# Kernel tuning notes

Hardware: AMD Instinct MI355X
Metric: run time of the kernel (lower is better)

Reference implementation:

```python
import jax, jax.numpy as jnp
import numpy as np
from jax import lax

HEADS, DIM_HEAD, KSZ = 8, 64, 3


def conv1x1(x, w):
    # x: [B, Cin, X, Y], w: [Cout, Cin]
    return jnp.einsum('oi,bixy->boxy', w, x)


def setup_inputs() -> dict:
    key = jax.random.key(0)
    ks = jax.random.split(key, 8)
    dim = 256
    inner = HEADS * DIM_HEAD  # 512
    B, H, W = 4, 64, 64
    s = 0.02
    return {
        'fmap': jax.random.normal(ks[0], (B, dim, H, W), jnp.float32),
        'w_lin_q': jax.random.normal(ks[1], (inner, dim), jnp.float32) * s,
        'w_lin_kv_dw': jax.random.normal(ks[2], (dim, 1, 3, 3), jnp.float32) * s,
        'w_lin_kv_pw': jax.random.normal(ks[3], (2 * inner, dim), jnp.float32) * s,
        'w_q': jax.random.normal(ks[4], (inner, dim), jnp.float32) * s,
        'w_kv': jax.random.normal(ks[5], (2 * inner, dim), jnp.float32) * s,
        'w_out': jax.random.normal(ks[6], (dim, 2 * inner), jnp.float32) * s,
        'b_out': jax.random.normal(ks[7], (dim,), jnp.float32) * s,
    }


def reference(fmap, w_lin_q, w_lin_kv_dw, w_lin_kv_pw, w_q, w_kv, w_out, b_out):
    B, dim, X, Y = fmap.shape
    h, d, ksz = HEADS, DIM_HEAD, KSZ
    scale = d ** -0.5
    n = X * Y

    # ---- linear (global) attention branch ----
    # depthwise 3x3 conv (groups=dim) then pointwise 1x1, both bias-free
    dw = lax.conv_general_dilated(
        fmap, w_lin_kv_dw, window_strides=(1, 1), padding=[(1, 1), (1, 1)],
        dimension_numbers=('NCHW', 'OIHW', 'NCHW'), feature_group_count=dim)
    lin_kv = conv1x1(dw, w_lin_kv_pw)
    lin_q = conv1x1(fmap, w_lin_q)
    lin_k, lin_v = jnp.split(lin_kv, 2, axis=1)

    def to_bhnd(t):  # [B, h*d, X, Y] -> [B, h, n, d]
        return t.reshape(B, h, d, n).transpose(0, 1, 3, 2)

    lq, lk, lv = to_bhnd(lin_q), to_bhnd(lin_k), to_bhnd(lin_v)
    lq = jax.nn.softmax(lq, axis=-1) * scale   # softmax over feature dim
    lk = jax.nn.softmax(lk, axis=-2)           # softmax over sequence dim
    ctx = jnp.einsum('bhnd,bhne->bhde', lk, lv)
    lin_out = jnp.einsum('bhnd,bhde->bhne', lq, ctx)
    lin_out = lin_out.transpose(0, 1, 3, 2).reshape(B, h * d, X, Y)
    lin_out = jax.nn.gelu(lin_out, approximate=False)  # torch nn.GELU (exact erf)

    # ---- local window attention branch (unfold equivalent) ----
    q = conv1x1(fmap, w_q).reshape(B, h, d, X, Y) * scale
    kv = conv1x1(fmap, w_kv)
    k, v = jnp.split(kv, 2, axis=1)
    k = k.reshape(B, h, d, X, Y)
    v = v.reshape(B, h, d, X, Y)
    pad = ksz // 2
    padw = ((0, 0), (0, 0), (0, 0), (pad, pad), (pad, pad))
    kp = jnp.pad(k, padw)  # zero padding, as in F.unfold
    vp = jnp.pad(v, padw)
    # j enumerates kernel offsets row-major (ky, kx) -> matches F.unfold layout
    k_win = jnp.stack([kp[..., i:i + X, j:j + Y]
                       for i in range(ksz) for j in range(ksz)], axis=2)  # [B,h,j,d,X,Y]
    v_win = jnp.stack([vp[..., i:i + X, j:j + Y]
                       for i in range(ksz) for j in range(ksz)], axis=2)
    sim = jnp.einsum('bhdxy,bhjdxy->bhxyj', q, k_win)
    attn = jax.nn.softmax(sim, axis=-1)  # stable (max-subtracted internally)
    full = jnp.einsum('bhxyj,bhjdxy->bhdxy', attn, v_win)
    full = full.reshape(B, h * d, X, Y)

    out = jnp.concatenate([lin_out, full], axis=1)  # [B, 2*inner, X, Y]
    return conv1x1(out, w_out) + b_out[None, :, None, None]
```

## Files before the change

kernel.cpp:

```cpp
#include <hip/hip_runtime.h>
#include <cmath>

#define NPIX 4096
#define NTOT 16384
#define CIN  256

typedef __bf16 bf16x8 __attribute__((ext_vector_type(8)));
typedef float  f32x4  __attribute__((ext_vector_type(4)));
typedef unsigned short u16x8 __attribute__((ext_vector_type(8)));

static __device__ __forceinline__ unsigned short f2bf(float f) {
    unsigned u = __float_as_uint(f);
    unsigned r = (u + 0x7FFFu + ((u >> 16) & 1u)) >> 16;
    return (unsigned short)r;
}
static __device__ __forceinline__ float bf2f(unsigned short u) {
    return __uint_as_float((unsigned)u << 16);
}

__global__ __launch_bounds__(256) void k_transpose_bf(const float* __restrict__ src,
                                                      unsigned short* __restrict__ dst) {
    __shared__ float tile[64][65];
    int p0 = blockIdx.x * 64;
    int c0 = blockIdx.y * 64;
    int b  = blockIdx.z;
    int t = threadIdx.x;
    int tp = t & 63, tg = t >> 6;
    const float* s = src + ((size_t)(b * 256 + c0) * 4096) + p0;
#pragma unroll
    for (int r = 0; r < 16; ++r) {
        int c = r * 4 + tg;
        tile[tp][c] = s[(size_t)c * 4096 + tp];
    }
    __syncthreads();
    unsigned short* d = dst + ((size_t)(b * 4096 + p0)) * 256 + c0;
#pragma unroll
    for (int r = 0; r < 16; ++r) {
        int pr = r * 4 + tg;
        d[(size_t)pr * 256 + tp] = f2bf(tile[pr][tp]);
    }
}

__global__ __launch_bounds__(256) void k_dwconv_bf(const unsigned short* __restrict__ FMB,
                                                   const float* __restrict__ wdw,
                                                   unsigned short* __restrict__ DWB) {
    __shared__ float wl[2560];
    int t = threadIdx.x;
    for (int i = t; i < 2304; i += 256) wl[(i / 9) * 10 + (i % 9)] = wdw[i];
    __syncthreads();
    int idx = blockIdx.x * 256 + t;
    int cg = idx & 31, p = idx >> 5;
    int xy = p & 4095, x = xy >> 6, y = xy & 63;
    const unsigned short* base = FMB + (size_t)p * 256 + cg * 8;
    float s[8] = {0.f, 0.f, 0.f, 0.f, 0.f, 0.f, 0.f, 0.f};
#pragma unroll
    for (int dx = 0; dx < 3; ++dx) {
        int xx = x + dx - 1;
        if ((unsigned)xx >= 64u) continue;
#pragma unroll
        for (int dy = 0; dy < 3; ++dy) {
            int yy = y + dy - 1;
            if ((unsigned)yy >= 64u) continue;
            u16x8 v = *(const u16x8*)(base + ((dx - 1) * 64 + (dy - 1)) * 256);
#pragma unroll
            for (int d = 0; d < 8; ++d)
                s[d] += bf2f(v[d]) * wl[(cg * 8 + d) * 10 + dx * 3 + dy];
        }
    }
    uint4 w0;
    w0.x = (unsigned)f2bf(s[0]) | ((unsigned)f2bf(s[1]) << 16);
    w0.y = (unsigned)f2bf(s[2]) | ((unsigned)f2bf(s[3]) << 16);
    w0.z = (unsigned)f2bf(s[4]) | ((unsigned)f2bf(s[5]) << 16);
    w0.w = (unsigned)f2bf(s[6]) | ((unsigned)f2bf(s[7]) << 16);
    *(uint4*)(DWB + (size_t)p * 256 + cg * 8) = w0;
}

__global__ __launch_bounds__(256) void k_convert_w(const float* __restrict__ w1, const float* __restrict__ w2,
                                                   const float* __restrict__ w3, const float* __restrict__ w4,
                                                   const float* __restrict__ w5,
                                                   unsigned short* __restrict__ dst) {
    int i = blockIdx.x * 256 + threadIdx.x;
    float v;
    if (i < 131072)       v = w1[i];
    else if (i < 262144)  v = w2[i - 131072];
    else if (i < 524288)  v = w3[i - 262144];
    else if (i < 786432) {
        int elem = i - 524288;
        int rp = elem >> 8, c = elem & 255;
        int h = rp >> 7, wi = rp & 127;
        int srow = (wi < 64) ? (h * 64 + wi) : (512 + h * 64 + (wi - 64));
        v = w4[srow * 256 + c];
    } else                v = w5[i - 786432];
    dst[i] = f2bf(v);
}

__global__ __launch_bounds__(256) void k_qkv_gemm(const __bf16* __restrict__ FMB,
                                                  const __bf16* __restrict__ DWB,
                                                  const __bf16* __restrict__ WQKV,
                                                  const __bf16* __restrict__ WPW,
                                                  unsigned short* __restrict__ LQB,
                                                  unsigned short* __restrict__ CKV2,
                                                  float* __restrict__ ctx,
                                                  float* __restrict__ S) {
    __shared__ __align__(16) __bf16 SMEM[128 * 136];
    __bf16* As = SMEM;
    __bf16* Bs = SMEM + 128 * 64;
    const int K = 256;
    const int m0 = blockIdx.x * 128;
    const int by = blockIdx.y;
    const bool g2 = (by >= 16);
    const __bf16* A = g2 ? DWB : FMB;
    const __bf16* B = g2 ? WPW : WQKV;
    const int n0 = (g2 ? by - 16 : by) * 128;
    const int t = threadIdx.x;
    const int w = t >> 6, l = t & 63;
    const int wm = (w >> 1) * 64, wn = (w & 1) * 64;
    f32x4 acc[4][4];
#pragma unroll
    for (int i = 0; i < 4; ++i)
#pragma unroll
        for (int j = 0; j < 4; ++j) acc[i][j] = (f32x4){0.f, 0.f, 0.f, 0.f};

    const int lrow = l >> 3;
    const int lchunk = (l & 7) ^ lrow;
    for (int k0 = 0; k0 < K; k0 += 64) {
#pragma unroll
        for (int r = 0; r < 4; ++r) {
            const int s = w + r * 4;
            const int row = s * 8 + lrow;
            const __bf16* ga = A + (size_t)(m0 + row) * K + (k0 + lchunk * 8);
            const __bf16* gb = B + (size_t)(n0 + row) * K + (k0 + lchunk * 8);
            __builtin_amdgcn_global_load_lds((const __attribute__((address_space(1))) void*)ga,
                                             (__attribute__((address_space(3))) void*)(As + s * 512),
                                             16, 0, 0);
            __builtin_amdgcn_global_load_lds((const __attribute__((address_space(1))) void*)gb,
                                             (__attribute__((address_space(3))) void*)(Bs + s * 512),
                                             16, 0, 0);
        }
        __syncthreads();
#pragma unroll
        for (int ks = 0; ks < 2; ++ks) {
            bf16x8 af[4], bfr[4];
#pragma unroll
            for (int i = 0; i < 4; ++i) {
                const int arow = wm + i * 16 + (l & 15);
                const int ac = ((l >> 4) + ks * 4) ^ (l & 7);
                af[i] = *(const bf16x8*)(As + arow * 64 + ac * 8);
                const int brow = wn + i * 16 + (l & 15);
                bfr[i] = *(const bf16x8*)(Bs + brow * 64 + ac * 8);
            }
#pragma unroll
            for (int i = 0; i < 4; ++i)
#pragma unroll
                for (int j = 0; j < 4; ++j)
                    acc[i][j] = __builtin_amdgcn_mfma_f32_16x16x32_bf16(af[i], bfr[j], acc[i][j], 0, 0, 0);
        }
        __syncthreads();
    }

    if (g2) {
        unsigned short* ST = (unsigned short*)SMEM;
#pragma unroll
        for (int i = 0; i < 4; ++i) {
            const int prow = wm + i * 16 + (l >> 4) * 4;
#pragma unroll
            for (int j = 0; j < 4; ++j) {
                const int col = wn + j * 16 + (l & 15);
#pragma unroll
                for (int q = 0; q < 4; ++q) {
                    float v = acc[i][j][q];
                    ST[col * 130 + prow + q] = f2bf(col < 64 ? __expf(v) : v);
                }
            }
        }
        __syncthreads();
        const int h  = n0 >> 7;
        const int bh = (m0 >> 12) * 8 + h;
        const int dm = (w >> 1) * 32, en = (w & 1) * 32;
        f32x4 c2[2][2];
        f32x4 s2[2];
#pragma unroll
        for (int i = 0; i < 2; ++i) {
            s2[i] = (f32x4){0.f, 0.f, 0.f, 0.f};
#pragma unroll
            for (int j = 0; j < 2; ++j) c2[i][j] = (f32x4){0.f, 0.f, 0.f, 0.f};
        }
        bf16x8 ones;
#pragma unroll
        for (int d = 0; d < 8; ++d) ones[d] = (__bf16)1.0f;
#pragma unroll
        for (int kp = 0; kp < 4; ++kp) {
            bf16x8 af2[2], bv2[2];
#pragma unroll
            for (int i = 0; i < 2; ++i) {
                const int drow = dm + i * 16 + (l & 15);
                af2[i] = *(const bf16x8*)(ST + drow * 130 + kp * 32 + (l >> 4) * 8);
                const int erow = 64 + en + i * 16 + (l & 15);
                bv2[i] = *(const bf16x8*)(ST + erow * 130 + kp * 32 + (l >> 4) * 8);
            }
#pragma unroll
            for (int i = 0; i < 2; ++i)
#pragma unroll
                for (int j = 0; j < 2; ++j)
                    c2[i][j] = __builtin_amdgcn_mfma_f32_16x16x32_bf16(af2[i], bv2[j], c2[i][j], 0, 0, 0);
            if ((w & 1) == 0)
#pragma unroll
                for (int i = 0; i < 2; ++i)
                    s2[i] = __builtin_amdgcn_mfma_f32_16x16x32_bf16(af2[i], ones, s2[i], 0, 0, 0);
        }
        float* ctxh = ctx + (size_t)bh * 4096;
#pragma unroll
        for (int i = 0; i < 2; ++i)
#pragma unroll
            for (int j = 0; j < 2; ++j) {
                const int e = en + j * 16 + (l & 15);
#pragma unroll
                for (int q = 0; q < 4; ++q) {
                    const int d = dm + i * 16 + (l >> 4) * 4 + q;
                    atomicAdd(&ctxh[d * 64 + e], c2[i][j][q]);
                }
            }
        if ((w & 1) == 0 && (l & 15) == 0) {
#pragma unroll
            for (int i = 0; i < 2; ++i)
#pragma unroll
                for (int q = 0; q < 4; ++q)
                    atomicAdd(&S[bh * 64 + dm + i * 16 + (l >> 4) * 4 + q], s2[i][q]);
        }
        return;
    }

#pragma unroll
    for (int i = 0; i < 4; ++i) {
        const int prow = wm + i * 16 + (l >> 4) * 4;
#pragma unroll
        for (int j = 0; j < 4; ++j) {
            const int col = wn + j * 16 + (l & 15);
            const int cglob = n0 + col;
            const float sc = (cglob >= 512 && cglob < 1024) ? 0.125f : 1.f;
#pragma unroll
            for (int q = 0; q < 4; ++q)
                *((unsigned short*)SMEM + (prow + q) * 136 + col) = f2bf(acc[i][j][q] * sc);
        }
    }
    __syncthreads();
    const int pix = t >> 1, half = t & 1;
    const unsigned short* sp = (const unsigned short*)SMEM + pix * 136 + half * 64;
    if (n0 < 512) {
        float m = -1e30f;
#pragma unroll
        for (int r = 0; r < 8; ++r) {
            u16x8 v = *(const u16x8*)(sp + r * 8);
#pragma unroll
            for (int d = 0; d < 8; ++d) m = fmaxf(m, bf2f(v[d]));
        }
        float Z = 0.f;
#pragma unroll
        for (int r = 0; r < 8; ++r) {
            u16x8 v = *(const u16x8*)(sp + r * 8);
#pragma unroll
            for (int d = 0; d < 8; ++d) Z += __expf(bf2f(v[d]) - m);
        }
        float inv = 0.125f / Z;
        unsigned short* dst = LQB + (size_t)(m0 + pix) * 512 + n0 + half * 64;
#pragma unroll
        for (int r = 0; r < 8; ++r) {
            u16x8 v = *(const u16x8*)(sp + r * 8);
            float o[8];
#pragma unroll
            for (int d = 0; d < 8; ++d) o[d] = __expf(bf2f(v[d]) - m) * inv;
            uint4 wv;
            wv.x = (unsigned)f2bf(o[0]) | ((unsigned)f2bf(o[1]) << 16);
            wv.y = (unsigned)f2bf(o[2]) | ((unsigned)f2bf(o[3]) << 16);
            wv.z = (unsigned)f2bf(o[4]) | ((unsigned)f2bf(o[5]) << 16);
            wv.w = (unsigned)f2bf(o[6]) | ((unsigned)f2bf(o[7]) << 16);
            *(uint4*)(dst + r * 8) = wv;
        }
    } else {
        unsigned short* dptr = CKV2 + (size_t)(m0 + pix) * 1536 + (n0 - 512) + half * 64;
#pragma unroll
        for (int r = 0; r < 8; ++r)
            *(u16x8*)(dptr + r * 8) = *(const u16x8*)(sp + r * 8);
    }
}

__global__ __launch_bounds__(256) void k_out_gemm(const __bf16* __restrict__ A,
                                                  const __bf16* __restrict__ B,
                                                  float* __restrict__ C,
                                                  const float* __restrict__ bias) {
    __shared__ __align__(16) __bf16 SMEM[32768];
    const int K = 1024;
    const int m0 = blockIdx.x * 128, n0 = blockIdx.y * 128;
    const int t = threadIdx.x;
    const int w = t >> 6, l = t & 63;
    const int wm = (w >> 1) * 64, wn = (w & 1) * 64;
    f32x4 acc[4][4];
#pragma unroll
    for (int i = 0; i < 4; ++i)
#pragma unroll
        for (int j = 0; j < 4; ++j) acc[i][j] = (f32x4){0.f, 0.f, 0.f, 0.f};

    const int lrow = l >> 3;
    const int lchunk = (l & 7) ^ lrow;
    auto stage = [&](int buf, int k0) {
        __bf16* As = SMEM + buf * 16384;
        __bf16* Bs = As + 8192;
#pragma unroll
        for (int r = 0; r < 4; ++r) {
            const int s = w + r * 4;
            const int row = s * 8 + lrow;
            const __bf16* ga = A + (size_t)(m0 + row) * K + (k0 + lchunk * 8);
            const __bf16* gb = B + (size_t)(n0 + row) * K + (k0 + lchunk * 8);
            __builtin_amdgcn_global_load_lds((const __attribute__((address_space(1))) void*)ga,
                                             (__attribute__((address_space(3))) void*)(As + s * 512),
                                             16, 0, 0);
            __builtin_amdgcn_global_load_lds((const __attribute__((address_space(1))) void*)gb,
                                             (__attribute__((address_space(3))) void*)(Bs + s * 512),
                                             16, 0, 0);
        }
    };

    stage(0, 0);
    for (int it = 0; it < 16; ++it) {
        __syncthreads();
        if (it < 15) stage((it + 1) & 1, (it + 1) * 64);
        const __bf16* As = SMEM + (it & 1) * 16384;
        const __bf16* Bs = As + 8192;
#pragma unroll
        for (int ks = 0; ks < 2; ++ks) {
            bf16x8 af[4], bfr[4];
#pragma unroll
            for (int i = 0; i < 4; ++i) {
                const int arow = wm + i * 16 + (l & 15);
                const int ac = ((l >> 4) + ks * 4) ^ (l & 7);
                af[i] = *(const bf16x8*)(As + arow * 64 + ac * 8);
                const int brow = wn + i * 16 + (l & 15);
                bfr[i] = *(const bf16x8*)(Bs + brow * 64 + ac * 8);
            }
#pragma unroll
            for (int i = 0; i < 4; ++i)
#pragma unroll
                for (int j = 0; j < 4; ++j)
                    acc[i][j] = __builtin_amdgcn_mfma_f32_16x16x32_bf16(af[i], bfr[j], acc[i][j], 0, 0, 0);
        }
    }
    const int b = m0 >> 12;
#pragma unroll
    for (int j = 0; j < 4; ++j) {
        const int col = n0 + wn + j * 16 + (l & 15);
        const float bv = bias[col];
        float* obase = C + ((size_t)(b * 256 + col) << 12);
#pragma unroll
        for (int i = 0; i < 4; ++i) {
            const int rb = (m0 & 4095) + wm + i * 16 + (l >> 4) * 4;
            f32x4 v = acc[i][j];
            v[0] += bv; v[1] += bv; v[2] += bv; v[3] += bv;
            *(f32x4*)(obase + rb) = v;
        }
    }
}

__global__ __launch_bounds__(256) void k_ctxnorm(const float* __restrict__ ctx,
                                                 const float* __restrict__ S,
                                                 unsigned short* __restrict__ ctxb) {
    int bh = blockIdx.x;
    __shared__ float sinv[64];
    int t = threadIdx.x;
    if (t < 64) sinv[t] = 1.f / S[bh * 64 + t];
    __syncthreads();
    const float* src = ctx + (size_t)bh * 4096;
    unsigned short* dst = ctxb + (size_t)bh * 4096;
#pragma unroll
    for (int i = t; i < 4096; i += 256) {
        int d = i & 63, e = i >> 6;
        dst[i] = f2bf(src[d * 64 + e] * sinv[d]);
    }
}

__global__ __launch_bounds__(256) void k_lin_mfma(const __bf16* __restrict__ LQB,
                                                  const __bf16* __restrict__ ctxb,
                                                  unsigned short* __restrict__ CAT) {
    const int p0 = blockIdx.x * 128;
    const int h  = blockIdx.y;
    const int b  = p0 >> 12;
    const int t = threadIdx.x, w = t >> 6, l = t & 63;
    const int wm = w * 32;
    const __bf16* Bm = ctxb + (size_t)(b * 8 + h) * 4096;
    f32x4 acc[2][4];
#pragma unroll
    for (int i = 0; i < 2; ++i)
#pragma unroll
        for (int j = 0; j < 4; ++j) acc[i][j] = (f32x4){0.f, 0.f, 0.f, 0.f};
#pragma unroll
    for (int ks = 0; ks < 2; ++ks) {
        const int c = (l >> 4) + ks * 4;
        bf16x8 af[2], bfr[4];
#pragma unroll
        for (int i = 0; i < 2; ++i) {
            const int row = p0 + wm + i * 16 + (l & 15);
            af[i] = *(const bf16x8*)(LQB + (size_t)row * 512 + h * 64 + c * 8);
        }
#pragma unroll
        for (int j = 0; j < 4; ++j) {
            const int erow = j * 16 + (l & 15);
            bfr[j] = *(const bf16x8*)(Bm + erow * 64 + c * 8);
        }
#pragma unroll
        for (int i = 0; i < 2; ++i)
#pragma unroll
            for (int j = 0; j < 4; ++j)
                acc[i][j] = __builtin_amdgcn_mfma_f32_16x16x32_bf16(af[i], bfr[j], acc[i][j], 0, 0, 0);
    }
#pragma unroll
    for (int i = 0; i < 2; ++i) {
#pragma unroll
        for (int j = 0; j < 4; ++j) {
            const int e = j * 16 + (l & 15);
#pragma unroll
            for (int q = 0; q < 4; ++q) {
                const int p = p0 + wm + i * 16 + (l >> 4) * 4 + q;
                float x = acc[i][j][q];
                float g = 0.5f * x * (1.f + erff(x * 0.70710678118654752f));
                CAT[(size_t)p * 1024 + h * 64 + e] = f2bf(g);
            }
        }
    }
}

__global__ __launch_bounds__(256) void k_local_attn(const unsigned short* __restrict__ CKV,
                                                    unsigned short* __restrict__ CAT) {
    const int W = blockIdx.x * 4 + (threadIdx.x >> 6);
    const int lane = threadIdx.x & 63;
    const int h = W & 7;
    const int G = W >> 3;
    const int yg = G & 7, x = (G >> 3) & 63, b = G >> 9;
    const int lg = lane >> 3, c8 = lane & 7;
    const int y = (yg << 3) + lg;
    const int p = (b << 12) + (x << 6) + y;
    const unsigned short* Qp = CKV + (size_t)p * 1536 + h * 64 + c8 * 8;
    const unsigned short* Kp = Qp + 512;
    const unsigned short* Vp = Qp + 1024;

    const bool okx[3] = {x > 0, true, x < 63};
    const bool oky[3] = {y > 0, true, y < 63};
    bool okn[9]; int ofs[9];
#pragma unroll
    for (int dx = 0; dx < 3; ++dx)
#pragma unroll
        for (int dy = 0; dy < 3; ++dy) {
            const int k = dx * 3 + dy;
            okn[k] = okx[dx] && oky[dy];
            ofs[k] = okn[k] ? ((dx - 1) * 64 + (dy - 1)) * 1536 : 0;
        }
    float qf[8];
    {
        u16x8 q8 = *(const u16x8*)Qp;
#pragma unroll
        for (int d = 0; d < 8; ++d) qf[d] = bf2f(q8[d]);
    }
    float sim[9];
#pragma unroll
    for (int k = 0; k < 9; ++k) {
        u16x8 k8 = *(const u16x8*)(Kp + ofs[k]);
        float s = 0.f;
#pragma unroll
        for (int d = 0; d < 8; ++d) s += qf[d] * bf2f(k8[d]);
        s = okn[k] ? s : 0.f;
        s += __shfl_xor(s, 1);
        s += __shfl_xor(s, 2);
        s += __shfl_xor(s, 4);
        sim[k] = s;
    }
    float mx = sim[0];
#pragma unroll
    for (int k = 1; k < 9; ++k) mx = fmaxf(mx, sim[k]);
    float a[9], Z = 0.f;
#pragma unroll
    for (int k = 0; k < 9; ++k) { a[k] = __expf(sim[k] - mx); Z += a[k]; }
    float inv = 1.f / Z;
#pragma unroll
    for (int k = 0; k < 9; ++k) a[k] = okn[k] ? a[k] * inv : 0.f;
    float o[8] = {0.f, 0.f, 0.f, 0.f, 0.f, 0.f, 0.f, 0.f};
#pragma unroll
    for (int k = 0; k < 9; ++k) {
        u16x8 v8 = *(const u16x8*)(Vp + ofs[k]);
#pragma unroll
        for (int d = 0; d < 8; ++d) o[d] += a[k] * bf2f(v8[d]);
    }
    unsigned short* dst = CAT + (size_t)p * 1024 + 512 + h * 64 + c8 * 8;
    uint4 w0;
    w0.x = (unsigned)f2bf(o[0]) | ((unsigned)f2bf(o[1]) << 16);
    w0.y = (unsigned)f2bf(o[2]) | ((unsigned)f2bf(o[3]) << 16);
    w0.z = (unsigned)f2bf(o[4]) | ((unsigned)f2bf(o[5]) << 16);
    w0.w = (unsigned)f2bf(o[6]) | ((unsigned)f2bf(o[7]) << 16);
    *(uint4*)dst = w0;
}

extern "C" void kernel_launch(void* const* d_in, const int* in_sizes, int n_in,
                              void* d_out, int out_size, void* d_ws, size_t ws_size,
                              hipStream_t stream) {
    const float* fmap  = (const float*)d_in[0];
    const float* w_lq  = (const float*)d_in[1];
    const float* w_dw  = (const float*)d_in[2];
    const float* w_pw  = (const float*)d_in[3];
    const float* w_q   = (const float*)d_in[4];
    const float* w_kv  = (const float*)d_in[5];
    const float* w_out = (const float*)d_in[6];
    const float* b_out = (const float*)d_in[7];
    float* out = (float*)d_out;

    unsigned short* base = (unsigned short*)d_ws;
    unsigned short* CATB = base;
    unsigned short* FMB  = base + (size_t)NTOT * 1024;
    unsigned short* DWB  = FMB + (size_t)NTOT * 256;
    unsigned short* WB   = DWB + (size_t)NTOT * 256;
    unsigned short* WQKV = WB;
    unsigned short* WPW  = WB + 524288;
    unsigned short* WOUT = WB + 786432;
    unsigned short* CTXB = WB + 1048576;
    unsigned short* LQB  = CTXB + 131072;
    unsigned short* CKV2 = LQB + (size_t)NTOT * 512;
    float* ctx = (float*)(CKV2 + (size_t)NTOT * 1536);
    float* S   = ctx + 32 * 4096;

    k_transpose_bf<<<dim3(64, 4, 4), 256, 0, stream>>>(fmap, FMB);
    k_convert_w<<<4096, 256, 0, stream>>>(w_lq, w_q, w_kv, w_pw, w_out, WB);
    hipMemsetAsync(ctx, 0, (size_t)(32 * 4096 + 2048) * sizeof(float), stream);
    k_dwconv_bf<<<2048, 256, 0, stream>>>(FMB, w_dw, DWB);
    k_qkv_gemm<<<dim3(128, 24), 256, 0, stream>>>((const __bf16*)FMB, (const __bf16*)DWB,
                                                  (const __bf16*)WQKV, (const __bf16*)WPW,
                                                  LQB, CKV2, ctx, S);
    k_ctxnorm<<<32, 256, 0, stream>>>(ctx, S, CTXB);
    k_lin_mfma<<<dim3(128, 8), 256, 0, stream>>>((const __bf16*)LQB, (const __bf16*)CTXB, CATB);
    k_local_attn<<<4096, 256, 0, stream>>>(CKV2, CATB);
    k_out_gemm<<<dim3(128, 2), 256, 0, stream>>>((const __bf16*)CATB, (const __bf16*)WOUT, out, b_out);
}
```

Measured before the change: 173.5 us.

## Widen QKV GEMM tile to 128x256 with two-pass epilogue

New measurement: 172.4 us. About the same (-0.6%).

```diff
diff --git a/kernel.cpp b/kernel.cpp
--- a/kernel.cpp
+++ b/kernel.cpp
@@ -94,32 +94,32 @@
     dst[i] = f2bf(v);
 }
 
-__global__ __launch_bounds__(256) void k_qkv_gemm(const __bf16* __restrict__ FMB,
-                                                  const __bf16* __restrict__ DWB,
-                                                  const __bf16* __restrict__ WQKV,
-                                                  const __bf16* __restrict__ WPW,
-                                                  unsigned short* __restrict__ LQB,
-                                                  unsigned short* __restrict__ CKV2,
-                                                  float* __restrict__ ctx,
-                                                  float* __restrict__ S) {
-    __shared__ __align__(16) __bf16 SMEM[128 * 136];
+__global__ __launch_bounds__(256, 2) void k_qkv_gemm(const __bf16* __restrict__ FMB,
+                                                     const __bf16* __restrict__ DWB,
+                                                     const __bf16* __restrict__ WQKV,
+                                                     const __bf16* __restrict__ WPW,
+                                                     unsigned short* __restrict__ LQB,
+                                                     unsigned short* __restrict__ CKV2,
+                                                     float* __restrict__ ctx,
+                                                     float* __restrict__ S) {
+    __shared__ __align__(16) __bf16 SMEM[24576];
     __bf16* As = SMEM;
-    __bf16* Bs = SMEM + 128 * 64;
+    __bf16* Bs = SMEM + 8192;
     const int K = 256;
     const int m0 = blockIdx.x * 128;
     const int by = blockIdx.y;
-    const bool g2 = (by >= 16);
+    const bool g2 = (by >= 8);
     const __bf16* A = g2 ? DWB : FMB;
     const __bf16* B = g2 ? WPW : WQKV;
-    const int n0 = (g2 ? by - 16 : by) * 128;
+    const int n0 = (g2 ? by - 8 : by) * 256;
     const int t = threadIdx.x;
     const int w = t >> 6, l = t & 63;
-    const int wm = (w >> 1) * 64, wn = (w & 1) * 64;
-    f32x4 acc[4][4];
+    const int wm = (w >> 1) * 64, wn = (w & 1) * 128;
+    f32x4 acc[4][8];
 #pragma unroll
     for (int i = 0; i < 4; ++i)
 #pragma unroll
-        for (int j = 0; j < 4; ++j) acc[i][j] = (f32x4){0.f, 0.f, 0.f, 0.f};
+        for (int j = 0; j < 8; ++j) acc[i][j] = (f32x4){0.f, 0.f, 0.f, 0.f};
 
     const int lrow = l >> 3;
     const int lchunk = (l & 7) ^ lrow;
@@ -129,10 +129,15 @@
             const int s = w + r * 4;
             const int row = s * 8 + lrow;
             const __bf16* ga = A + (size_t)(m0 + row) * K + (k0 + lchunk * 8);
-            const __bf16* gb = B + (size_t)(n0 + row) * K + (k0 + lchunk * 8);
             __builtin_amdgcn_global_load_lds((const __attribute__((address_space(1))) void*)ga,
                                              (__attribute__((address_space(3))) void*)(As + s * 512),
                                              16, 0, 0);
+        }
+#pragma unroll
+        for (int r = 0; r < 8; ++r) {
+            const int s = w + r * 4;
+            const int row = s * 8 + lrow;
+            const __bf16* gb = B + (size_t)(n0 + row) * K + (k0 + lchunk * 8);
             __builtin_amdgcn_global_load_lds((const __attribute__((address_space(1))) void*)gb,
                                              (__attribute__((address_space(3))) void*)(Bs + s * 512),
                                              16, 0, 0);
@@ -140,147 +145,158 @@
         __syncthreads();
 #pragma unroll
         for (int ks = 0; ks < 2; ++ks) {
-            bf16x8 af[4], bfr[4];
+            const int ac = ((l >> 4) + ks * 4) ^ (l & 7);
+            bf16x8 af[4], bfr[8];
 #pragma unroll
             for (int i = 0; i < 4; ++i) {
                 const int arow = wm + i * 16 + (l & 15);
-                const int ac = ((l >> 4) + ks * 4) ^ (l & 7);
                 af[i] = *(const bf16x8*)(As + arow * 64 + ac * 8);
-                const int brow = wn + i * 16 + (l & 15);
-                bfr[i] = *(const bf16x8*)(Bs + brow * 64 + ac * 8);
+            }
+#pragma unroll
+            for (int j = 0; j < 8; ++j) {
+                const int brow = wn + j * 16 + (l & 15);
+                bfr[j] = *(const bf16x8*)(Bs + brow * 64 + ac * 8);
             }
 #pragma unroll
             for (int i = 0; i < 4; ++i)
 #pragma unroll
-                for (int j = 0; j < 4; ++j)
+                for (int j = 0; j < 8; ++j)
                     acc[i][j] = __builtin_amdgcn_mfma_f32_16x16x32_bf16(af[i], bfr[j], acc[i][j], 0, 0, 0);
         }
         __syncthreads();
     }
 
-    if (g2) {
-        unsigned short* ST = (unsigned short*)SMEM;
-#pragma unroll
-        for (int i = 0; i < 4; ++i) {
-            const int prow = wm + i * 16 + (l >> 4) * 4;
-#pragma unroll
-            for (int j = 0; j < 4; ++j) {
-                const int col = wn + j * 16 + (l & 15);
-#pragma unroll
-                for (int q = 0; q < 4; ++q) {
-                    float v = acc[i][j][q];
-                    ST[col * 130 + prow + q] = f2bf(col < 64 ? __expf(v) : v);
+    unsigned short* SU = (unsigned short*)SMEM;
+#pragma unroll
+    for (int pass = 0; pass < 2; ++pass) {
+        if ((w & 1) == pass) {
+            if (!g2) {
+#pragma unroll
+                for (int i = 0; i < 4; ++i) {
+                    const int prow = wm + i * 16 + (l >> 4) * 4;
+#pragma unroll
+                    for (int j = 0; j < 8; ++j) {
+                        const int col = j * 16 + (l & 15);
+                        const int cglob = n0 + pass * 128 + col;
+                        const float sc = (cglob >= 512 && cglob < 1024) ? 0.125f : 1.f;
+#pragma unroll
+                        for (int q = 0; q < 4; ++q)
+                            SU[(prow + q) * 136 + col] = f2bf(acc[i][j][q] * sc);
+                    }
+                }
+            } else {
+#pragma unroll
+                for (int i = 0; i < 4; ++i) {
+                    const int prow = wm + i * 16 + (l >> 4) * 4;
+#pragma unroll
+                    for (int j = 0; j < 8; ++j) {
+                        const int col = j * 16 + (l & 15);
+#pragma unroll
+                        for (int q = 0; q < 4; ++q) {
+                            float v = acc[i][j][q];
+                            SU[col * 130 + prow + q] = f2bf(col < 64 ? __expf(v) : v);
+                        }
+                    }
                 }
             }
         }
         __syncthreads();
-        const int h  = n0 >> 7;
-        const int bh = (m0 >> 12) * 8 + h;
-        const int dm = (w >> 1) * 32, en = (w & 1) * 32;
-        f32x4 c2[2][2];
-        f32x4 s2[2];
-#pragma unroll
-        for (int i = 0; i < 2; ++i) {
-            s2[i] = (f32x4){0.f, 0.f, 0.f, 0.f};
-#pragma unroll
-            for (int j = 0; j < 2; ++j) c2[i][j] = (f32x4){0.f, 0.f, 0.f, 0.f};
-        }
-        bf16x8 ones;
-#pragma unroll
-        for (int d = 0; d < 8; ++d) ones[d] = (__bf16)1.0f;
-#pragma unroll
-        for (int kp = 0; kp < 4; ++kp) {
-            bf16x8 af2[2], bv2[2];
+        if (!g2) {
+            const int pix = t >> 1, half = t & 1;
+            const unsigned short* sp = SU + pix * 136 + half * 64;
+            const int cg0 = n0 + pass * 128 + half * 64;
+            if (cg0 < 512) {
+                float m = -1e30f;
+#pragma unroll
+                for (int r = 0; r < 8; ++r) {
+                    u16x8 v = *(const u16x8*)(sp + r * 8);
+#pragma unroll
+                    for (int d = 0; d < 8; ++d) m = fmaxf(m, bf2f(v[d]));
+                }
+                float Z = 0.f;
+#pragma unroll
+                for (int r = 0; r < 8; ++r) {
+                    u16x8 v = *(const u16x8*)(sp + r * 8);
+#pragma unroll
+                    for (int d = 0; d < 8; ++d) Z += __expf(bf2f(v[d]) - m);
+                }
+                float inv = 0.125f / Z;
+                unsigned short* dst = LQB + (size_t)(m0 + pix) * 512 + cg0;
+#pragma unroll
+                for (int r = 0; r < 8; ++r) {
+                    u16x8 v = *(const u16x8*)(sp + r * 8);
+                    float o[8];
+#pragma unroll
+                    for (int d = 0; d < 8; ++d) o[d] = __expf(bf2f(v[d]) - m) * inv;
+                    uint4 wv;
+                    wv.x = (unsigned)f2bf(o[0]) | ((unsigned)f2bf(o[1]) << 16);
+                    wv.y = (unsigned)f2bf(o[2]) | ((unsigned)f2bf(o[3]) << 16);
+                    wv.z = (unsigned)f2bf(o[4]) | ((unsigned)f2bf(o[5]) << 16);
+                    wv.w = (unsigned)f2bf(o[6]) | ((unsigned)f2bf(o[7]) << 16);
+                    *(uint4*)(dst + r * 8) = wv;
+                }
+            } else {
+                unsigned short* dptr = CKV2 + (size_t)(m0 + pix) * 1536 + (cg0 - 512);
+#pragma unroll
+                for (int r = 0; r < 8; ++r)
+                    *(u16x8*)(dptr + r * 8) = *(const u16x8*)(sp + r * 8);
+            }
+        } else {
+            const int h  = (n0 + pass * 128) >> 7;
+            const int bh = (m0 >> 12) * 8 + h;
+            const int dm = (w >> 1) * 32, en = (w & 1) * 32;
+            f32x4 c2[2][2];
+            f32x4 s2[2];
 #pragma unroll
             for (int i = 0; i < 2; ++i) {
-                const int drow = dm + i * 16 + (l & 15);
-                af2[i] = *(const bf16x8*)(ST + drow * 130 + kp * 32 + (l >> 4) * 8);
-                const int erow = 64 + en + i * 16 + (l & 15);
-                bv2[i] = *(const bf16x8*)(ST + erow * 130 + kp * 32 + (l >> 4) * 8);
-            }
+                s2[i] = (f32x4){0.f, 0.f, 0.f, 0.f};
+#pragma unroll
+                for (int j = 0; j < 2; ++j) c2[i][j] = (f32x4){0.f, 0.f, 0.f, 0.f};
+            }
+            bf16x8 ones;
+#pragma unroll
+            for (int d = 0; d < 8; ++d) ones[d] = (__bf16)1.0f;
+#pragma unroll
+            for (int kp = 0; kp < 4; ++kp) {
+                bf16x8 af2[2], bv2[2];
+#pragma unroll
+                for (int i = 0; i < 2; ++i) {
+                    const int drow = dm + i * 16 + (l & 15);
+                    af2[i] = *(const bf16x8*)(SU + drow * 130 + kp * 32 + (l >> 4) * 8);
+                    const int erow = 64 + en + i * 16 + (l & 15);
+                    bv2[i] = *(const bf16x8*)(SU + erow * 130 + kp * 32 + (l >> 4) * 8);
+                }
+#pragma unroll
+                for (int i = 0; i < 2; ++i)
+#pragma unroll
+                    for (int j = 0; j < 2; ++j)
+                        c2[i][j] = __builtin_amdgcn_mfma_f32_16x16x32_bf16(af2[i], bv2[j], c2[i][j], 0, 0, 0);
+                if ((w & 1) == 0)
+#pragma unroll
+                    for (int i = 0; i < 2; ++i)
+                        s2[i] = __builtin_amdgcn_mfma_f32_16x16x32_bf16(af2[i], ones, s2[i], 0, 0, 0);
+            }
+            float* ctxh = ctx + (size_t)bh * 4096;
 #pragma unroll
             for (int i = 0; i < 2; ++i)
 #pragma unroll
-                for (int j = 0; j < 2; ++j)
-                    c2[i][j] = __builtin_amdgcn_mfma_f32_16x16x32_bf16(af2[i], bv2[j], c2[i][j], 0, 0, 0);
-            if ((w & 1) == 0)
+                for (int j = 0; j < 2; ++j) {
+                    const int e = en + j * 16 + (l & 15);
+#pragma unroll
+                    for (int q = 0; q < 4; ++q) {
+                        const int d = dm + i * 16 + (l >> 4) * 4 + q;
+                        atomicAdd(&ctxh[d * 64 + e], c2[i][j][q]);
+                    }
+                }
+            if ((w & 1) == 0 && (l & 15) == 0) {
 #pragma unroll
                 for (int i = 0; i < 2; ++i)
-                    s2[i] = __builtin_amdgcn_mfma_f32_16x16x32_bf16(af2[i], ones, s2[i], 0, 0, 0);
-        }
-        float* ctxh = ctx + (size_t)bh * 4096;
-#pragma unroll
-        for (int i = 0; i < 2; ++i)
-#pragma unroll
-            for (int j = 0; j < 2; ++j) {
-                const int e = en + j * 16 + (l & 15);
-#pragma unroll
-                for (int q = 0; q < 4; ++q) {
-                    const int d = dm + i * 16 + (l >> 4) * 4 + q;
-                    atomicAdd(&ctxh[d * 64 + e], c2[i][j][q]);
-                }
-            }
-        if ((w & 1) == 0 && (l & 15) == 0) {
-#pragma unroll
-            for (int i = 0; i < 2; ++i)
-#pragma unroll
-                for (int q = 0; q < 4; ++q)
-                    atomicAdd(&S[bh * 64 + dm + i * 16 + (l >> 4) * 4 + q], s2[i][q]);
-        }
-        return;
-    }
-
-#pragma unroll
-    for (int i = 0; i < 4; ++i) {
-        const int prow = wm + i * 16 + (l >> 4) * 4;
-#pragma unroll
-        for (int j = 0; j < 4; ++j) {
-            const int col = wn + j * 16 + (l & 15);
-            const int cglob = n0 + col;
-            const float sc = (cglob >= 512 && cglob < 1024) ? 0.125f : 1.f;
-#pragma unroll
-            for (int q = 0; q < 4; ++q)
-                *((unsigned short*)SMEM + (prow + q) * 136 + col) = f2bf(acc[i][j][q] * sc);
-        }
-    }
-    __syncthreads();
-    const int pix = t >> 1, half = t & 1;
-    const unsigned short* sp = (const unsigned short*)SMEM + pix * 136 + half * 64;
-    if (n0 < 512) {
-        float m = -1e30f;
-#pragma unroll
-        for (int r = 0; r < 8; ++r) {
-            u16x8 v = *(const u16x8*)(sp + r * 8);
-#pragma unroll
-            for (int d = 0; d < 8; ++d) m = fmaxf(m, bf2f(v[d]));
-        }
-        float Z = 0.f;
-#pragma unroll
-        for (int r = 0; r < 8; ++r) {
-            u16x8 v = *(const u16x8*)(sp + r * 8);
-#pragma unroll
-            for (int d = 0; d < 8; ++d) Z += __expf(bf2f(v[d]) - m);
-        }
-        float inv = 0.125f / Z;
-        unsigned short* dst = LQB + (size_t)(m0 + pix) * 512 + n0 + half * 64;
-#pragma unroll
-        for (int r = 0; r < 8; ++r) {
-            u16x8 v = *(const u16x8*)(sp + r * 8);
-            float o[8];
-#pragma unroll
-            for (int d = 0; d < 8; ++d) o[d] = __expf(bf2f(v[d]) - m) * inv;
-            uint4 wv;
-            wv.x = (unsigned)f2bf(o[0]) | ((unsigned)f2bf(o[1]) << 16);
-            wv.y = (unsigned)f2bf(o[2]) | ((unsigned)f2bf(o[3]) << 16);
-            wv.z = (unsigned)f2bf(o[4]) | ((unsigned)f2bf(o[5]) << 16);
-            wv.w = (unsigned)f2bf(o[6]) | ((unsigned)f2bf(o[7]) << 16);
-            *(uint4*)(dst + r * 8) = wv;
-        }
-    } else {
-        unsigned short* dptr = CKV2 + (size_t)(m0 + pix) * 1536 + (n0 - 512) + half * 64;
-#pragma unroll
-        for (int r = 0; r < 8; ++r)
-            *(u16x8*)(dptr + r * 8) = *(const u16x8*)(sp + r * 8);
+#pragma unroll
+                    for (int q = 0; q < 4; ++q)
+                        atomicAdd(&S[bh * 64 + dm + i * 16 + (l >> 4) * 4 + q], s2[i][q]);
+            }
+        }
+        __syncthreads();
     }
 }
 
@@ -527,7 +543,7 @@
     k_convert_w<<<4096, 256, 0, stream>>>(w_lq, w_q, w_kv, w_pw, w_out, WB);
     hipMemsetAsync(ctx, 0, (size_t)(32 * 4096 + 2048) * sizeof(float), stream);
     k_dwconv_bf<<<2048, 256, 0, stream>>>(FMB, w_dw, DWB);
-    k_qkv_gemm<<<dim3(128, 24), 256, 0, stream>>>((const __bf16*)FMB, (const __bf16*)DWB,
+    k_qkv_gemm<<<dim3(128, 12), 256, 0, stream>>>((const __bf16*)FMB, (const __bf16*)DWB,
                                                   (const __bf16*)WQKV, (const __bf16*)WPW,
                                                   LQB, CKV2, ctx, S);
     k_ctxnorm<<<32, 256, 0, stream>>>(ctx, S, CTXB);
```

## Replace ctx atomics with partial buffers and halve out-GEMM M tile

Applied to the files above, without the earlier changes.

New measurement: 166.0 us. -4.3%, faster.

```diff
diff --git a/kernel.cpp b/kernel.cpp
--- a/kernel.cpp
+++ b/kernel.cpp
@@ -100,7 +100,7 @@
                                                   const __bf16* __restrict__ WPW,
                                                   unsigned short* __restrict__ LQB,
                                                   unsigned short* __restrict__ CKV2,
-                                                  float* __restrict__ ctx,
+                                                  float* __restrict__ PART,
                                                   float* __restrict__ S) {
     __shared__ __align__(16) __bf16 SMEM[128 * 136];
     __bf16* As = SMEM;
@@ -208,18 +208,12 @@
                 for (int i = 0; i < 2; ++i)
                     s2[i] = __builtin_amdgcn_mfma_f32_16x16x32_bf16(af2[i], ones, s2[i], 0, 0, 0);
         }
-        float* ctxh = ctx + (size_t)bh * 4096;
+        float* pp = PART + ((size_t)((m0 >> 7) * 8 + h)) * 4096 + t * 16;
 #pragma unroll
         for (int i = 0; i < 2; ++i)
 #pragma unroll
-            for (int j = 0; j < 2; ++j) {
-                const int e = en + j * 16 + (l & 15);
-#pragma unroll
-                for (int q = 0; q < 4; ++q) {
-                    const int d = dm + i * 16 + (l >> 4) * 4 + q;
-                    atomicAdd(&ctxh[d * 64 + e], c2[i][j][q]);
-                }
-            }
+            for (int j = 0; j < 2; ++j)
+                *(f32x4*)(pp + (i * 2 + j) * 4) = c2[i][j];
         if ((w & 1) == 0 && (l & 15) == 0) {
 #pragma unroll
             for (int i = 0; i < 2; ++i)
@@ -284,36 +278,74 @@
     }
 }
 
+__global__ __launch_bounds__(256) void k_ctxnorm(const float* __restrict__ PART,
+                                                 const float* __restrict__ S,
+                                                 unsigned short* __restrict__ ctxb) {
+    __shared__ float SUM[1024];
+    __shared__ float sinv[32];
+    const int bh = blockIdx.x, wq = blockIdx.y;
+    const int b = bh >> 3, h = bh & 7;
+    const int t = threadIdx.x;
+    const int bd = (wq >> 1) * 32, be = (wq & 1) * 32;
+#pragma unroll
+    for (int r = 0; r < 4; ++r) {
+        const int kl = t + 256 * r;
+        const float* src = PART + (size_t)((b * 32) * 8 + h) * 4096 + wq * 1024 + kl;
+        float s = 0.f;
+#pragma unroll
+        for (int mi = 0; mi < 32; ++mi)
+            s += src[(size_t)mi * 8 * 4096];
+        SUM[kl] = s;
+    }
+    if (t < 32) sinv[t] = 1.f / S[bh * 64 + bd + t];
+    __syncthreads();
+#pragma unroll
+    for (int r = 0; r < 4; ++r) {
+        const int idx = t + 256 * r;
+        const int dd = idx & 31, ee = idx >> 5;
+        const int d = bd + dd, e = be + ee;
+        const int l2 = (((d >> 2) & 3) << 4) | (e & 15);
+        const int i2 = (d >> 4) & 1, j2 = (e >> 4) & 1, q = d & 3;
+        const int kl = l2 * 16 + (i2 * 2 + j2) * 4 + q;
+        ctxb[(size_t)bh * 4096 + e * 64 + d] = f2bf(SUM[kl] * sinv[dd]);
+    }
+}
+
 __global__ __launch_bounds__(256) void k_out_gemm(const __bf16* __restrict__ A,
                                                   const __bf16* __restrict__ B,
                                                   float* __restrict__ C,
                                                   const float* __restrict__ bias) {
-    __shared__ __align__(16) __bf16 SMEM[32768];
+    __shared__ __align__(16) __bf16 SMEM[24576];
     const int K = 1024;
-    const int m0 = blockIdx.x * 128, n0 = blockIdx.y * 128;
+    const int m0 = blockIdx.x * 64, n0 = blockIdx.y * 128;
     const int t = threadIdx.x;
     const int w = t >> 6, l = t & 63;
-    const int wm = (w >> 1) * 64, wn = (w & 1) * 64;
-    f32x4 acc[4][4];
-#pragma unroll
-    for (int i = 0; i < 4; ++i)
+    const int wm = (w >> 1) * 32, wn = (w & 1) * 64;
+    f32x4 acc[2][4];
+#pragma unroll
+    for (int i = 0; i < 2; ++i)
 #pragma unroll
         for (int j = 0; j < 4; ++j) acc[i][j] = (f32x4){0.f, 0.f, 0.f, 0.f};
 
     const int lrow = l >> 3;
     const int lchunk = (l & 7) ^ lrow;
     auto stage = [&](int buf, int k0) {
-        __bf16* As = SMEM + buf * 16384;
-        __bf16* Bs = As + 8192;
+        __bf16* As = SMEM + buf * 12288;
+        __bf16* Bs = As + 4096;
+#pragma unroll
+        for (int r = 0; r < 2; ++r) {
+            const int s = w + r * 4;
+            const int row = s * 8 + lrow;
+            const __bf16* ga = A + (size_t)(m0 + row) * K + (k0 + lchunk * 8);
+            __builtin_amdgcn_global_load_lds((const __attribute__((address_space(1))) void*)ga,
+                                             (__attribute__((address_space(3))) void*)(As + s * 512),
+                                             16, 0, 0);
+        }
 #pragma unroll
         for (int r = 0; r < 4; ++r) {
             const int s = w + r * 4;
             const int row = s * 8 + lrow;
-            const __bf16* ga = A + (size_t)(m0 + row) * K + (k0 + lchunk * 8);
             const __bf16* gb = B + (size_t)(n0 + row) * K + (k0 + lchunk * 8);
-            __builtin_amdgcn_global_load_lds((const __attribute__((address_space(1))) void*)ga,
-                                             (__attribute__((address_space(3))) void*)(As + s * 512),
-                                             16, 0, 0);
             __builtin_amdgcn_global_load_lds((const __attribute__((address_space(1))) void*)gb,
                                              (__attribute__((address_space(3))) void*)(Bs + s * 512),
                                              16, 0, 0);
@@ -324,21 +356,24 @@
     for (int it = 0; it < 16; ++it) {
         __syncthreads();
         if (it < 15) stage((it + 1) & 1, (it + 1) * 64);
-        const __bf16* As = SMEM + (it & 1) * 16384;
-        const __bf16* Bs = As + 8192;
+        const __bf16* As = SMEM + (it & 1) * 12288;
+        const __bf16* Bs = As + 4096;
 #pragma unroll
         for (int ks = 0; ks < 2; ++ks) {
-            bf16x8 af[4], bfr[4];
-#pragma unroll
-            for (int i = 0; i < 4; ++i) {
+            const int ac = ((l >> 4) + ks * 4) ^ (l & 7);
+            bf16x8 af[2], bfr[4];
+#pragma unroll
+            for (int i = 0; i < 2; ++i) {
                 const int arow = wm + i * 16 + (l & 15);
-                const int ac = ((l >> 4) + ks * 4) ^ (l & 7);
                 af[i] = *(const bf16x8*)(As + arow * 64 + ac * 8);
-                const int brow = wn + i * 16 + (l & 15);
-                bfr[i] = *(const bf16x8*)(Bs + brow * 64 + ac * 8);
             }
 #pragma unroll
-            for (int i = 0; i < 4; ++i)
+            for (int j = 0; j < 4; ++j) {
+                const int brow = wn + j * 16 + (l & 15);
+                bfr[j] = *(const bf16x8*)(Bs + brow * 64 + ac * 8);
+            }
+#pragma unroll
+            for (int i = 0; i < 2; ++i)
 #pragma unroll
                 for (int j = 0; j < 4; ++j)
                     acc[i][j] = __builtin_amdgcn_mfma_f32_16x16x32_bf16(af[i], bfr[j], acc[i][j], 0, 0, 0);
@@ -351,29 +386,12 @@
         const float bv = bias[col];
         float* obase = C + ((size_t)(b * 256 + col) << 12);
 #pragma unroll
-        for (int i = 0; i < 4; ++i) {
+        for (int i = 0; i < 2; ++i) {
             const int rb = (m0 & 4095) + wm + i * 16 + (l >> 4) * 4;
             f32x4 v = acc[i][j];
             v[0] += bv; v[1] += bv; v[2] += bv; v[3] += bv;
             *(f32x4*)(obase + rb) = v;
         }
-    }
-}
-
-__global__ __launch_bounds__(256) void k_ctxnorm(const float* __restrict__ ctx,
-                                                 const float* __restrict__ S,
-                                                 unsigned short* __restrict__ ctxb) {
-    int bh = blockIdx.x;
-    __shared__ float sinv[64];
-    int t = threadIdx.x;
-    if (t < 64) sinv[t] = 1.f / S[bh * 64 + t];
-    __syncthreads();
-    const float* src = ctx + (size_t)bh * 4096;
-    unsigned short* dst = ctxb + (size_t)bh * 4096;
-#pragma unroll
-    for (int i = t; i < 4096; i += 256) {
-        int d = i & 63, e = i >> 6;
-        dst[i] = f2bf(src[d * 64 + e] * sinv[d]);
     }
 }
 
@@ -520,18 +538,18 @@
     unsigned short* CTXB = WB + 1048576;
     unsigned short* LQB  = CTXB + 131072;
     unsigned short* CKV2 = LQB + (size_t)NTOT * 512;
-    float* ctx = (float*)(CKV2 + (size_t)NTOT * 1536);
-    float* S   = ctx + 32 * 4096;
+    float* PART = (float*)(CKV2 + (size_t)NTOT * 1536);
+    float* S    = PART + (size_t)1024 * 4096;
 
     k_transpose_bf<<<dim3(64, 4, 4), 256, 0, stream>>>(fmap, FMB);
     k_convert_w<<<4096, 256, 0, stream>>>(w_lq, w_q, w_kv, w_pw, w_out, WB);
-    hipMemsetAsync(ctx, 0, (size_t)(32 * 4096 + 2048) * sizeof(float), stream);
+    hipMemsetAsync(S, 0, 2048 * sizeof(float), stream);
     k_dwconv_bf<<<2048, 256, 0, stream>>>(FMB, w_dw, DWB);
     k_qkv_gemm<<<dim3(128, 24), 256, 0, stream>>>((const __bf16*)FMB, (const __bf16*)DWB,
                                                   (const __bf16*)WQKV, (const __bf16*)WPW,
-                                                  LQB, CKV2, ctx, S);
-    k_ctxnorm<<<32, 256, 0, stream>>>(ctx, S, CTXB);
+                                                  LQB, CKV2, PART, S);
+    k_ctxnorm<<<dim3(32, 4), 256, 0, stream>>>(PART, S, CTXB);
     k_lin_mfma<<<dim3(128, 8), 256, 0, stream>>>((const __bf16*)LQB, (const __bf16*)CTXB, CATB);
     k_local_attn<<<4096, 256, 0, stream>>>(CKV2, CATB);
-    k_out_gemm<<<dim3(128, 2), 256, 0, stream>>>((const __bf16*)CATB, (const __bf16*)WOUT, out, b_out);
-}
+    k_out_gemm<<<dim3(256, 2), 256, 0, stream>>>((const __bf16*)CATB, (const __bf16*)WOUT, out, b_out);
+}
```
